# Optimization experiments

Hardware: AMD Instinct MI355X
Metric: run time of the kernel (lower is better)

The kernel has to match this reference:

```python
import jax, jax.numpy as jnp
import numpy as np
import math

N, S, D, V = 8, 2048, 64, 64

def setup_inputs() -> dict:
    key = jax.random.key(0)
    k1, k2, k3, k4 = jax.random.split(key, 4)
    return {
        "queries_nqd": jax.random.normal(k1, (N, S, D), dtype=jnp.float32),
        "keys_nsd": jax.random.normal(k2, (N, S, D), dtype=jnp.float32),
        "values_nsv": jax.random.normal(k3, (N, S, V), dtype=jnp.float32),
        "prefix_len_n": jax.random.randint(k4, (N,), 0, S, dtype=jnp.int64) if jax.config.jax_enable_x64 else jax.random.randint(k4, (N,), 0, S, dtype=jnp.int32),
    }

def reference(queries_nqd, keys_nsd, values_nsv, prefix_len_n):
    n, q, d = queries_nqd.shape
    s = keys_nsd.shape[1]
    # block mask: key position < prefix_len (broadcast over query dim)  [n, q, s]
    s_idx = jnp.arange(s)
    block_mask = s_idx[None, None, :] < prefix_len_n[:, None, None]
    # diagonal mask: q == s index  [q, s]
    diag_mask = s_idx[:, None] == s_idx[None, :]
    attention_mask_nqs = block_mask | diag_mask[None, :, :]
    scores_nqs = jnp.einsum("nqd,nsd->nqs", queries_nqd, keys_nsd) / math.sqrt(d)
    scores_nqs = jnp.where(attention_mask_nqs, scores_nqs, jnp.float32(-1e9))
    probs_nqs = jax.nn.softmax(scores_nqs, axis=-1)
    # dropout p=0.0 (eval/identity)
    return jnp.einsum("nqs,nsv->nqv", probs_nqs, values_nsv)
```

## Files before the change

kernel.cpp:

```cpp
#include <hip/hip_runtime.h>
#include <cstdint>
#include <cstddef>

typedef __attribute__((ext_vector_type(8))) __bf16 bf16x8;
typedef __attribute__((ext_vector_type(2))) __bf16 bf16x2;
typedef __attribute__((ext_vector_type(4))) float f32x4;
typedef __attribute__((ext_vector_type(4))) unsigned int u32x4;

#define LOG2E 1.44269504088896340736f

constexpr int N_ = 8;
constexpr int S_ = 2048;
constexpr int D_ = 64;
constexpr int V_ = 64;
constexpr int TQ = 16;
constexpr int CK = 64;
constexpr int NW = 4;

#define GLD(d, a, OFF) \
    asm volatile("global_load_dwordx4 %0, %1, off offset:" OFF : "=&v"(d) : "v"(a))
#define VDRAIN() do { asm volatile("s_waitcnt vmcnt(0)" ::: "memory"); \
                      __builtin_amdgcn_sched_barrier(0); } while (0)

__device__ __forceinline__ ushort f2bf(float x) {
    uint u = __builtin_bit_cast(uint, x);
    return (ushort)((u + 0x7FFFu + ((u >> 16) & 1u)) >> 16);
}
__device__ __forceinline__ bf16x8 bc8(const u32x4& q) {
    return __builtin_bit_cast(bf16x8, q);
}
__device__ __forceinline__ bf16x8 cvt8(const float* p, float sc) {
    f32x4 a = *reinterpret_cast<const f32x4*>(p);
    f32x4 b = *reinterpret_cast<const f32x4*>(p + 4);
    bf16x8 r;
#pragma unroll
    for (int j = 0; j < 4; j++) { r[j] = (__bf16)(a[j] * sc); r[j + 4] = (__bf16)(b[j] * sc); }
    return r;
}
__device__ __forceinline__ uint pk2(float lo, float hi) {
    bf16x2 t; t[0] = (__bf16)lo; t[1] = (__bf16)hi;
    return __builtin_bit_cast(uint, t);
}

__device__ __forceinline__ int load_prefix(const int* plen, int n) {
    bool is64 = ((plen[1] | plen[3] | plen[5] | plen[7]) == 0);
    return is64 ? plen[2 * n] : plen[n];
}

__global__ void prep_kernel(const float* __restrict__ Q, const float* __restrict__ K,
                            const float* __restrict__ V, ushort* __restrict__ Qb,
                            ushort* __restrict__ Kb, ushort* __restrict__ VTb) {
    const float QS = 0.125f * LOG2E;
    const int i4 = (blockIdx.x * 256 + threadIdx.x) * 4;
    f32x4 q = *reinterpret_cast<const f32x4*>(Q + i4);
    f32x4 k = *reinterpret_cast<const f32x4*>(K + i4);
    f32x4 v = *reinterpret_cast<const f32x4*>(V + i4);
    ushort4 qo, ko;
    qo.x = f2bf(q[0] * QS); qo.y = f2bf(q[1] * QS); qo.z = f2bf(q[2] * QS); qo.w = f2bf(q[3] * QS);
    ko.x = f2bf(k[0]); ko.y = f2bf(k[1]); ko.z = f2bf(k[2]); ko.w = f2bf(k[3]);
    *reinterpret_cast<ushort4*>(Qb + i4) = qo;
    *reinterpret_cast<ushort4*>(Kb + i4) = ko;
    const int vd = i4 & (V_ - 1);
    const int s  = (i4 >> 6) & (S_ - 1);
    const int n  = i4 >> 17;
    const size_t base = ((size_t)n * 64 + (s >> 5)) * 2048 + (s & 31);
#pragma unroll
    for (int j = 0; j < 4; j++)
        VTb[base + (size_t)(vd + j) * 32] = f2bf(v[j]);
}

template <bool WS>
__global__ __launch_bounds__(256, 2) void attn_kernel(
    const void* __restrict__ Qp, const void* __restrict__ Kp,
    const void* __restrict__ Vp, const ushort* __restrict__ VTb,
    const int* __restrict__ plen, float* __restrict__ outm)
{
    __shared__ float obuf[NW][TQ][V_ + 1];
    __shared__ float lbuf[NW][TQ];

    const int n    = blockIdx.y;
    const int q0   = blockIdx.x * TQ;
    const int tid  = threadIdx.x;
    const int w    = tid >> 6;
    const int lane = tid & 63;
    const int quad = lane >> 4;
    const int l16  = lane & 15;
    const int prefix = load_prefix(plen, n);
    const int qrow = q0 + l16;

    const int krow = ((l16 >> 2) << 3) + (l16 & 3);

    bf16x8 qf0, qf1;
    if (WS) {
        const ushort* qptr = (const ushort*)Qp + ((size_t)(n * S_ + qrow)) * D_ + quad * 8;
        uint4 u0 = *reinterpret_cast<const uint4*>(qptr);
        uint4 u1 = *reinterpret_cast<const uint4*>(qptr + 32);
        qf0 = __builtin_bit_cast(bf16x8, u0); qf1 = __builtin_bit_cast(bf16x8, u1);
    } else {
        const float* qptr = (const float*)Qp + ((size_t)(n * S_ + qrow)) * D_ + quad * 8;
        qf0 = cvt8(qptr, 0.125f * LOG2E); qf1 = cvt8(qptr + 32, 0.125f * LOG2E);
    }

    f32x4 oacc[4];
#pragma unroll
    for (int vb = 0; vb < 4; vb++) oacc[vb] = (f32x4){0.f, 0.f, 0.f, 0.f};
    float l_r = 0.f;

    const float* Kf = (const float*)Kp + (size_t)n * S_ * D_;
    const float* Vf = (const float*)Vp + (size_t)n * S_ * V_;

    const uint64_t kbase0 = (uint64_t)(uintptr_t)((const ushort*)Kp)
        + (size_t)n * S_ * D_ * 2 + (size_t)krow * 128 + quad * 16;
    const uint64_t vbase0 = (uint64_t)(uintptr_t)VTb
        + (size_t)n * 64 * 2048 * 2 + (size_t)l16 * 64 + quad * 16;

    auto issueKV = [&](u32x4* f, int c) {
        const uint64_t ka = kbase0 + (uint64_t)c * (CK * 128);
        const uint64_t kb = ka + 4096;
        const uint64_t va = vbase0 + (uint64_t)c * (2 * 4096);
        const uint64_t vb = va + 4096;
        GLD(f[0],  ka, "0");   GLD(f[1],  ka, "64");
        GLD(f[2],  ka, "512"); GLD(f[3],  ka, "576");
        GLD(f[4],  kb, "0");   GLD(f[5],  kb, "64");
        GLD(f[6],  kb, "512"); GLD(f[7],  kb, "576");
        GLD(f[8],  va, "0");   GLD(f[9],  va, "1024");
        GLD(f[10], va, "2048");GLD(f[11], va, "3072");
        GLD(f[12], vb, "0");   GLD(f[13], vb, "1024");
        GLD(f[14], vb, "2048");GLD(f[15], vb, "3072");
    };

    auto computeKV = [&](const u32x4* f, int kb, bool masked) {
        const f32x4 zero = (f32x4){0.f, 0.f, 0.f, 0.f};
        f32x4 s0 = __builtin_amdgcn_mfma_f32_16x16x32_bf16(bc8(f[0]), qf0, zero, 0, 0, 0);
        s0 = __builtin_amdgcn_mfma_f32_16x16x32_bf16(bc8(f[1]), qf1, s0, 0, 0, 0);
        f32x4 s1 = __builtin_amdgcn_mfma_f32_16x16x32_bf16(bc8(f[2]), qf0, zero, 0, 0, 0);
        s1 = __builtin_amdgcn_mfma_f32_16x16x32_bf16(bc8(f[3]), qf1, s1, 0, 0, 0);
        f32x4 s2 = __builtin_amdgcn_mfma_f32_16x16x32_bf16(bc8(f[4]), qf0, zero, 0, 0, 0);
        s2 = __builtin_amdgcn_mfma_f32_16x16x32_bf16(bc8(f[5]), qf1, s2, 0, 0, 0);
        f32x4 s3 = __builtin_amdgcn_mfma_f32_16x16x32_bf16(bc8(f[6]), qf0, zero, 0, 0, 0);
        s3 = __builtin_amdgcn_mfma_f32_16x16x32_bf16(bc8(f[7]), qf1, s3, 0, 0, 0);
        if (masked) {
#pragma unroll
            for (int r = 0; r < 4; r++) {
                const int k0 = kb + 8 * quad + r;
                s0[r] = (k0      < prefix || k0      == qrow) ? s0[r] : -1e30f;
                s1[r] = (k0 + 4  < prefix || k0 + 4  == qrow) ? s1[r] : -1e30f;
                s2[r] = (k0 + 32 < prefix || k0 + 32 == qrow) ? s2[r] : -1e30f;
                s3[r] = (k0 + 36 < prefix || k0 + 36 == qrow) ? s3[r] : -1e30f;
            }
        }
        float p0[4], p1[4], p2[4], p3[4];
#pragma unroll
        for (int r = 0; r < 4; r++) {
            p0[r] = __builtin_amdgcn_exp2f(s0[r]);
            p1[r] = __builtin_amdgcn_exp2f(s1[r]);
            p2[r] = __builtin_amdgcn_exp2f(s2[r]);
            p3[r] = __builtin_amdgcn_exp2f(s3[r]);
        }
        l_r += ((p0[0] + p0[1]) + (p0[2] + p0[3])) + ((p1[0] + p1[1]) + (p1[2] + p1[3]))
             + ((p2[0] + p2[1]) + (p2[2] + p2[3])) + ((p3[0] + p3[1]) + (p3[2] + p3[3]));
        uint4 pw0, pw1;
        pw0.x = pk2(p0[0], p0[1]); pw0.y = pk2(p0[2], p0[3]);
        pw0.z = pk2(p1[0], p1[1]); pw0.w = pk2(p1[2], p1[3]);
        pw1.x = pk2(p2[0], p2[1]); pw1.y = pk2(p2[2], p2[3]);
        pw1.z = pk2(p3[0], p3[1]); pw1.w = pk2(p3[2], p3[3]);
        const bf16x8 pB0 = __builtin_bit_cast(bf16x8, pw0);
        const bf16x8 pB1 = __builtin_bit_cast(bf16x8, pw1);
#pragma unroll
        for (int vb = 0; vb < 4; vb++) {
            oacc[vb] = __builtin_amdgcn_mfma_f32_16x16x32_bf16(bc8(f[8 + vb]),  pB0, oacc[vb], 0, 0, 0);
            oacc[vb] = __builtin_amdgcn_mfma_f32_16x16x32_bf16(bc8(f[12 + vb]), pB1, oacc[vb], 0, 0, 0);
        }
    };

    auto computeNW = [&](int kb, bool masked) {
        const f32x4 zero = (f32x4){0.f, 0.f, 0.f, 0.f};
        const float* kp = Kf + (size_t)(kb + krow) * D_ + quad * 8;
        bf16x8 k0a = cvt8(kp, 1.f),           k0b = cvt8(kp + 32, 1.f);
        bf16x8 k1a = cvt8(kp + 4 * D_, 1.f),  k1b = cvt8(kp + 4 * D_ + 32, 1.f);
        bf16x8 k2a = cvt8(kp + 32 * D_, 1.f), k2b = cvt8(kp + 32 * D_ + 32, 1.f);
        bf16x8 k3a = cvt8(kp + 36 * D_, 1.f), k3b = cvt8(kp + 36 * D_ + 32, 1.f);
        f32x4 s0 = __builtin_amdgcn_mfma_f32_16x16x32_bf16(k0a, qf0, zero, 0, 0, 0);
        s0 = __builtin_amdgcn_mfma_f32_16x16x32_bf16(k0b, qf1, s0, 0, 0, 0);
        f32x4 s1 = __builtin_amdgcn_mfma_f32_16x16x32_bf16(k1a, qf0, zero, 0, 0, 0);
        s1 = __builtin_amdgcn_mfma_f32_16x16x32_bf16(k1b, qf1, s1, 0, 0, 0);
        f32x4 s2 = __builtin_amdgcn_mfma_f32_16x16x32_bf16(k2a, qf0, zero, 0, 0, 0);
        s2 = __builtin_amdgcn_mfma_f32_16x16x32_bf16(k2b, qf1, s2, 0, 0, 0);
        f32x4 s3 = __builtin_amdgcn_mfma_f32_16x16x32_bf16(k3a, qf0, zero, 0, 0, 0);
        s3 = __builtin_amdgcn_mfma_f32_16x16x32_bf16(k3b, qf1, s3, 0, 0, 0);
        if (masked) {
#pragma unroll
            for (int r = 0; r < 4; r++) {
                const int k0 = kb + 8 * quad + r;
                s0[r] = (k0      < prefix || k0      == qrow) ? s0[r] : -1e30f;
                s1[r] = (k0 + 4  < prefix || k0 + 4  == qrow) ? s1[r] : -1e30f;
                s2[r] = (k0 + 32 < prefix || k0 + 32 == qrow) ? s2[r] : -1e30f;
                s3[r] = (k0 + 36 < prefix || k0 + 36 == qrow) ? s3[r] : -1e30f;
            }
        }
        float p0[4], p1[4], p2[4], p3[4];
#pragma unroll
        for (int r = 0; r < 4; r++) {
            p0[r] = __builtin_amdgcn_exp2f(s0[r]);
            p1[r] = __builtin_amdgcn_exp2f(s1[r]);
            p2[r] = __builtin_amdgcn_exp2f(s2[r]);
            p3[r] = __builtin_amdgcn_exp2f(s3[r]);
        }
        l_r += ((p0[0] + p0[1]) + (p0[2] + p0[3])) + ((p1[0] + p1[1]) + (p1[2] + p1[3]))
             + ((p2[0] + p2[1]) + (p2[2] + p2[3])) + ((p3[0] + p3[1]) + (p3[2] + p3[3]));
        uint4 pw0, pw1;
        pw0.x = pk2(p0[0], p0[1]); pw0.y = pk2(p0[2], p0[3]);
        pw0.z = pk2(p1[0], p1[1]); pw0.w = pk2(p1[2], p1[3]);
        pw1.x = pk2(p2[0], p2[1]); pw1.y = pk2(p2[2], p2[3]);
        pw1.z = pk2(p3[0], p3[1]); pw1.w = pk2(p3[2], p3[3]);
        const bf16x8 pB0 = __builtin_bit_cast(bf16x8, pw0);
        const bf16x8 pB1 = __builtin_bit_cast(bf16x8, pw1);
#pragma unroll
        for (int vb = 0; vb < 4; vb++) {
            bf16x8 vf0, vf1;
#pragma unroll
            for (int j = 0; j < 8; j++) {
                vf0[j] = (__bf16)Vf[(size_t)(kb + quad * 8 + j) * V_ + vb * 16 + l16];
                vf1[j] = (__bf16)Vf[(size_t)(kb + 32 + quad * 8 + j) * V_ + vb * 16 + l16];
            }
            oacc[vb] = __builtin_amdgcn_mfma_f32_16x16x32_bf16(vf0, pB0, oacc[vb], 0, 0, 0);
            oacc[vb] = __builtin_amdgcn_mfma_f32_16x16x32_bf16(vf1, pB1, oacc[vb], 0, 0, 0);
        }
    };

    const int nFull = prefix >> 6;
    const int nPC   = (prefix + CK - 1) >> 6;
    const int dc    = q0 >> 6;

    if (WS) {
        u32x4 bufA[16], bufB[16];
        int c = w;
        if (c < nFull) {
            issueKV(bufA, c);
            VDRAIN();
            for (;;) {
                int cn = c + NW;
                if (cn >= nFull) { computeKV(bufA, c * CK, false); break; }
                issueKV(bufB, cn);
                computeKV(bufA, c * CK, false);
                VDRAIN();
                c = cn; cn = c + NW;
                if (cn >= nFull) { computeKV(bufB, c * CK, false); break; }
                issueKV(bufA, cn);
                computeKV(bufB, c * CK, false);
                VDRAIN();
                c = cn;
            }
        }
        if (nPC > nFull && (nFull & (NW - 1)) == w) {
            issueKV(bufA, nFull); VDRAIN(); computeKV(bufA, nFull * CK, true);
        }
        if (dc >= nPC && (dc & (NW - 1)) == w) {
            issueKV(bufA, dc); VDRAIN(); computeKV(bufA, dc * CK, true);
        }
    } else {
        for (int c = w; c < nFull; c += NW) computeNW(c * CK, false);
        if (nPC > nFull && (nFull & (NW - 1)) == w) computeNW(nFull * CK, true);
        if (dc >= nPC && (dc & (NW - 1)) == w) computeNW(dc * CK, true);
    }

#pragma unroll
    for (int vb = 0; vb < 4; vb++)
#pragma unroll
        for (int r = 0; r < 4; r++)
            obuf[w][l16][vb * 16 + quad * 4 + r] = oacc[vb][r];
    l_r += __shfl_xor(l_r, 16, 64);
    l_r += __shfl_xor(l_r, 32, 64);
    if (quad == 0) lbuf[w][l16] = l_r;
    __syncthreads();

    const int row = tid >> 4;
    const int vd0 = (tid & 15) * 4;
    float lg = (lbuf[0][row] + lbuf[1][row]) + (lbuf[2][row] + lbuf[3][row]);
    float acc[4] = {0.f, 0.f, 0.f, 0.f};
#pragma unroll
    for (int ww = 0; ww < NW; ww++) {
#pragma unroll
        for (int i = 0; i < 4; i++) acc[i] += obuf[ww][row][vd0 + i];
    }
    const float inv = 1.f / lg;
    f32x4 o4 = (f32x4){acc[0] * inv, acc[1] * inv, acc[2] * inv, acc[3] * inv};
    *reinterpret_cast<f32x4*>(outm + ((size_t)(n * S_ + q0 + row)) * V_ + vd0) = o4;
}

extern "C" void kernel_launch(void* const* d_in, const int* in_sizes, int n_in,
                              void* d_out, int out_size, void* d_ws, size_t ws_size,
                              hipStream_t stream) {
    const float* Qf = (const float*)d_in[0];
    const float* Kf = (const float*)d_in[1];
    const float* Vf = (const float*)d_in[2];
    const int* plen = (const int*)d_in[3];
    float* outm = (float*)d_out;

    constexpr size_t ELEMS = (size_t)N_ * S_ * D_;
    const size_t need = 3 * ELEMS * sizeof(ushort);
    dim3 agrid(S_ / TQ, N_);

    if (ws_size >= need) {
        ushort* Qb  = (ushort*)d_ws;
        ushort* Kb  = Qb + ELEMS;
        ushort* VTb = Kb + ELEMS;
        prep_kernel<<<ELEMS / (256 * 4), 256, 0, stream>>>(Qf, Kf, Vf, Qb, Kb, VTb);
        attn_kernel<true><<<agrid, 256, 0, stream>>>(Qb, Kb, nullptr, VTb, plen, outm);
    } else {
        attn_kernel<false><<<agrid, 256, 0, stream>>>(Qf, Kf, Vf, nullptr, plen, outm);
    }
}
```

Measured before the change: 101.3 us.

## Process two query tiles per warp and overlap K/V loads with partial waits

Doubles the query tile to 32 rows so each warp runs two 16-row score/PV MFMA streams over the same K/V fragments. This halves K/V global traffic per query and halves the grid. It also replaces full vmcnt drains with partial waits (vmcnt 24/16), so V loads and the next chunk's prefetch can overlap the QK computation. In exchange, register pressure is higher, there are fewer blocks to balance the uneven prefix lengths, and a dead no-op loop is left in the fallback path.

```diff
diff --git a/kernel.cpp b/kernel.cpp
--- a/kernel.cpp
+++ b/kernel.cpp
@@ -13,13 +13,13 @@
 constexpr int S_ = 2048;
 constexpr int D_ = 64;
 constexpr int V_ = 64;
-constexpr int TQ = 16;
+constexpr int TQ = 32;
 constexpr int CK = 64;
 constexpr int NW = 4;
 
 #define GLD(d, a, OFF) \
     asm volatile("global_load_dwordx4 %0, %1, off offset:" OFF : "=&v"(d) : "v"(a))
-#define VDRAIN() do { asm volatile("s_waitcnt vmcnt(0)" ::: "memory"); \
+#define WAITV(N) do { asm volatile("s_waitcnt vmcnt(" #N ")" ::: "memory"); \
                       __builtin_amdgcn_sched_barrier(0); } while (0)
 
 __device__ __forceinline__ ushort f2bf(float x) {
@@ -86,25 +86,31 @@
     const int quad = lane >> 4;
     const int l16  = lane & 15;
     const int prefix = load_prefix(plen, n);
-    const int qrow = q0 + l16;
+    const int qrow0 = q0 + l16;
+    const int qrow1 = q0 + 16 + l16;
 
     const int krow = ((l16 >> 2) << 3) + (l16 & 3);
 
-    bf16x8 qf0, qf1;
+    bf16x8 qf00, qf01, qf10, qf11;
     if (WS) {
-        const ushort* qptr = (const ushort*)Qp + ((size_t)(n * S_ + qrow)) * D_ + quad * 8;
+        const ushort* qptr = (const ushort*)Qp + ((size_t)(n * S_ + qrow0)) * D_ + quad * 8;
         uint4 u0 = *reinterpret_cast<const uint4*>(qptr);
         uint4 u1 = *reinterpret_cast<const uint4*>(qptr + 32);
-        qf0 = __builtin_bit_cast(bf16x8, u0); qf1 = __builtin_bit_cast(bf16x8, u1);
+        uint4 u2 = *reinterpret_cast<const uint4*>(qptr + 16 * D_);
+        uint4 u3 = *reinterpret_cast<const uint4*>(qptr + 16 * D_ + 32);
+        qf00 = __builtin_bit_cast(bf16x8, u0); qf01 = __builtin_bit_cast(bf16x8, u1);
+        qf10 = __builtin_bit_cast(bf16x8, u2); qf11 = __builtin_bit_cast(bf16x8, u3);
     } else {
-        const float* qptr = (const float*)Qp + ((size_t)(n * S_ + qrow)) * D_ + quad * 8;
-        qf0 = cvt8(qptr, 0.125f * LOG2E); qf1 = cvt8(qptr + 32, 0.125f * LOG2E);
+        const float* qptr = (const float*)Qp + ((size_t)(n * S_ + qrow0)) * D_ + quad * 8;
+        qf00 = cvt8(qptr, 0.125f * LOG2E);            qf01 = cvt8(qptr + 32, 0.125f * LOG2E);
+        qf10 = cvt8(qptr + 16 * D_, 0.125f * LOG2E);  qf11 = cvt8(qptr + 16 * D_ + 32, 0.125f * LOG2E);
     }
-
-    f32x4 oacc[4];
-#pragma unroll
-    for (int vb = 0; vb < 4; vb++) oacc[vb] = (f32x4){0.f, 0.f, 0.f, 0.f};
-    float l_r = 0.f;
+    asm volatile("" : "+v"(qf00), "+v"(qf01), "+v"(qf10), "+v"(qf11));
+
+    f32x4 oa[4], ob[4];
+#pragma unroll
+    for (int vb = 0; vb < 4; vb++) { oa[vb] = (f32x4){0.f,0.f,0.f,0.f}; ob[vb] = (f32x4){0.f,0.f,0.f,0.f}; }
+    float l0 = 0.f, l1 = 0.f;
 
     const float* Kf = (const float*)Kp + (size_t)n * S_ * D_;
     const float* Vf = (const float*)Vp + (size_t)n * S_ * V_;
@@ -129,102 +135,88 @@
         GLD(f[14], vb, "2048");GLD(f[15], vb, "3072");
     };
 
-    auto computeKV = [&](const u32x4* f, int kb, bool masked) {
+    auto computeChunk = [&](const u32x4* f, int kb, bool masked, bool wait16) {
         const f32x4 zero = (f32x4){0.f, 0.f, 0.f, 0.f};
-        f32x4 s0 = __builtin_amdgcn_mfma_f32_16x16x32_bf16(bc8(f[0]), qf0, zero, 0, 0, 0);
-        s0 = __builtin_amdgcn_mfma_f32_16x16x32_bf16(bc8(f[1]), qf1, s0, 0, 0, 0);
-        f32x4 s1 = __builtin_amdgcn_mfma_f32_16x16x32_bf16(bc8(f[2]), qf0, zero, 0, 0, 0);
-        s1 = __builtin_amdgcn_mfma_f32_16x16x32_bf16(bc8(f[3]), qf1, s1, 0, 0, 0);
-        f32x4 s2 = __builtin_amdgcn_mfma_f32_16x16x32_bf16(bc8(f[4]), qf0, zero, 0, 0, 0);
-        s2 = __builtin_amdgcn_mfma_f32_16x16x32_bf16(bc8(f[5]), qf1, s2, 0, 0, 0);
-        f32x4 s3 = __builtin_amdgcn_mfma_f32_16x16x32_bf16(bc8(f[6]), qf0, zero, 0, 0, 0);
-        s3 = __builtin_amdgcn_mfma_f32_16x16x32_bf16(bc8(f[7]), qf1, s3, 0, 0, 0);
-        if (masked) {
+        uint4 pw0, pw1, pw2, pw3;
+        {
+            f32x4 s0 = __builtin_amdgcn_mfma_f32_16x16x32_bf16(bc8(f[0]), qf00, zero, 0, 0, 0);
+            s0 = __builtin_amdgcn_mfma_f32_16x16x32_bf16(bc8(f[1]), qf01, s0, 0, 0, 0);
+            f32x4 s1 = __builtin_amdgcn_mfma_f32_16x16x32_bf16(bc8(f[2]), qf00, zero, 0, 0, 0);
+            s1 = __builtin_amdgcn_mfma_f32_16x16x32_bf16(bc8(f[3]), qf01, s1, 0, 0, 0);
+            f32x4 s2 = __builtin_amdgcn_mfma_f32_16x16x32_bf16(bc8(f[4]), qf00, zero, 0, 0, 0);
+            s2 = __builtin_amdgcn_mfma_f32_16x16x32_bf16(bc8(f[5]), qf01, s2, 0, 0, 0);
+            f32x4 s3 = __builtin_amdgcn_mfma_f32_16x16x32_bf16(bc8(f[6]), qf00, zero, 0, 0, 0);
+            s3 = __builtin_amdgcn_mfma_f32_16x16x32_bf16(bc8(f[7]), qf01, s3, 0, 0, 0);
+            if (masked) {
+#pragma unroll
+                for (int r = 0; r < 4; r++) {
+                    const int k0 = kb + 8 * quad + r;
+                    s0[r] = (k0      < prefix || k0      == qrow0) ? s0[r] : -1e30f;
+                    s1[r] = (k0 + 4  < prefix || k0 + 4  == qrow0) ? s1[r] : -1e30f;
+                    s2[r] = (k0 + 32 < prefix || k0 + 32 == qrow0) ? s2[r] : -1e30f;
+                    s3[r] = (k0 + 36 < prefix || k0 + 36 == qrow0) ? s3[r] : -1e30f;
+                }
+            }
+            float p0[4], p1[4], p2[4], p3[4];
 #pragma unroll
             for (int r = 0; r < 4; r++) {
-                const int k0 = kb + 8 * quad + r;
-                s0[r] = (k0      < prefix || k0      == qrow) ? s0[r] : -1e30f;
-                s1[r] = (k0 + 4  < prefix || k0 + 4  == qrow) ? s1[r] : -1e30f;
-                s2[r] = (k0 + 32 < prefix || k0 + 32 == qrow) ? s2[r] : -1e30f;
-                s3[r] = (k0 + 36 < prefix || k0 + 36 == qrow) ? s3[r] : -1e30f;
-            }
-        }
-        float p0[4], p1[4], p2[4], p3[4];
-#pragma unroll
-        for (int r = 0; r < 4; r++) {
-            p0[r] = __builtin_amdgcn_exp2f(s0[r]);
-            p1[r] = __builtin_amdgcn_exp2f(s1[r]);
-            p2[r] = __builtin_amdgcn_exp2f(s2[r]);
-            p3[r] = __builtin_amdgcn_exp2f(s3[r]);
-        }
-        l_r += ((p0[0] + p0[1]) + (p0[2] + p0[3])) + ((p1[0] + p1[1]) + (p1[2] + p1[3]))
-             + ((p2[0] + p2[1]) + (p2[2] + p2[3])) + ((p3[0] + p3[1]) + (p3[2] + p3[3]));
-        uint4 pw0, pw1;
-        pw0.x = pk2(p0[0], p0[1]); pw0.y = pk2(p0[2], p0[3]);
-        pw0.z = pk2(p1[0], p1[1]); pw0.w = pk2(p1[2], p1[3]);
-        pw1.x = pk2(p2[0], p2[1]); pw1.y = pk2(p2[2], p2[3]);
-        pw1.z = pk2(p3[0], p3[1]); pw1.w = pk2(p3[2], p3[3]);
-        const bf16x8 pB0 = __builtin_bit_cast(bf16x8, pw0);
-        const bf16x8 pB1 = __builtin_bit_cast(bf16x8, pw1);
+                p0[r] = __builtin_amdgcn_exp2f(s0[r]);
+                p1[r] = __builtin_amdgcn_exp2f(s1[r]);
+                p2[r] = __builtin_amdgcn_exp2f(s2[r]);
+                p3[r] = __builtin_amdgcn_exp2f(s3[r]);
+            }
+            l0 += ((p0[0]+p0[1])+(p0[2]+p0[3])) + ((p1[0]+p1[1])+(p1[2]+p1[3]))
+                + ((p2[0]+p2[1])+(p2[2]+p2[3])) + ((p3[0]+p3[1])+(p3[2]+p3[3]));
+            pw0.x = pk2(p0[0], p0[1]); pw0.y = pk2(p0[2], p0[3]);
+            pw0.z = pk2(p1[0], p1[1]); pw0.w = pk2(p1[2], p1[3]);
+            pw1.x = pk2(p2[0], p2[1]); pw1.y = pk2(p2[2], p2[3]);
+            pw1.z = pk2(p3[0], p3[1]); pw1.w = pk2(p3[2], p3[3]);
+        }
+        {
+            f32x4 s0 = __builtin_amdgcn_mfma_f32_16x16x32_bf16(bc8(f[0]), qf10, zero, 0, 0, 0);
+            s0 = __builtin_amdgcn_mfma_f32_16x16x32_bf16(bc8(f[1]), qf11, s0, 0, 0, 0);
+            f32x4 s1 = __builtin_amdgcn_mfma_f32_16x16x32_bf16(bc8(f[2]), qf10, zero, 0, 0, 0);
+            s1 = __builtin_amdgcn_mfma_f32_16x16x32_bf16(bc8(f[3]), qf11, s1, 0, 0, 0);
+            f32x4 s2 = __builtin_amdgcn_mfma_f32_16x16x32_bf16(bc8(f[4]), qf10, zero, 0, 0, 0);
+            s2 = __builtin_amdgcn_mfma_f32_16x16x32_bf16(bc8(f[5]), qf11, s2, 0, 0, 0);
+            f32x4 s3 = __builtin_amdgcn_mfma_f32_16x16x32_bf16(bc8(f[6]), qf10, zero, 0, 0, 0);
+            s3 = __builtin_amdgcn_mfma_f32_16x16x32_bf16(bc8(f[7]), qf11, s3, 0, 0, 0);
+            if (masked) {
+#pragma unroll
+                for (int r = 0; r < 4; r++) {
+                    const int k0 = kb + 8 * quad + r;
+                    s0[r] = (k0      < prefix || k0      == qrow1) ? s0[r] : -1e30f;
+                    s1[r] = (k0 + 4  < prefix || k0 + 4  == qrow1) ? s1[r] : -1e30f;
+                    s2[r] = (k0 + 32 < prefix || k0 + 32 == qrow1) ? s2[r] : -1e30f;
+                    s3[r] = (k0 + 36 < prefix || k0 + 36 == qrow1) ? s3[r] : -1e30f;
+                }
+            }
+            float p0[4], p1[4], p2[4], p3[4];
+#pragma unroll
+            for (int r = 0; r < 4; r++) {
+                p0[r] = __builtin_amdgcn_exp2f(s0[r]);
+                p1[r] = __builtin_amdgcn_exp2f(s1[r]);
+                p2[r] = __builtin_amdgcn_exp2f(s2[r]);
+                p3[r] = __builtin_amdgcn_exp2f(s3[r]);
+            }
+            l1 += ((p0[0]+p0[1])+(p0[2]+p0[3])) + ((p1[0]+p1[1])+(p1[2]+p1[3]))
+                + ((p2[0]+p2[1])+(p2[2]+p2[3])) + ((p3[0]+p3[1])+(p3[2]+p3[3]));
+            pw2.x = pk2(p0[0], p0[1]); pw2.y = pk2(p0[2], p0[3]);
+            pw2.z = pk2(p1[0], p1[1]); pw2.w = pk2(p1[2], p1[3]);
+            pw3.x = pk2(p2[0], p2[1]); pw3.y = pk2(p2[2], p2[3]);
+            pw3.z = pk2(p3[0], p3[1]); pw3.w = pk2(p3[2], p3[3]);
+        }
+        if (wait16) WAITV(16);
+        const bf16x8 pA0 = __builtin_bit_cast(bf16x8, pw0);
+        const bf16x8 pA1 = __builtin_bit_cast(bf16x8, pw1);
+        const bf16x8 pB0 = __builtin_bit_cast(bf16x8, pw2);
+        const bf16x8 pB1 = __builtin_bit_cast(bf16x8, pw3);
 #pragma unroll
         for (int vb = 0; vb < 4; vb++) {
-            oacc[vb] = __builtin_amdgcn_mfma_f32_16x16x32_bf16(bc8(f[8 + vb]),  pB0, oacc[vb], 0, 0, 0);
-            oacc[vb] = __builtin_amdgcn_mfma_f32_16x16x32_bf16(bc8(f[12 + vb]), pB1, oacc[vb], 0, 0, 0);
-        }
-    };
-
-    auto computeNW = [&](int kb, bool masked) {
-        const f32x4 zero = (f32x4){0.f, 0.f, 0.f, 0.f};
-        const float* kp = Kf + (size_t)(kb + krow) * D_ + quad * 8;
-        bf16x8 k0a = cvt8(kp, 1.f),           k0b = cvt8(kp + 32, 1.f);
-        bf16x8 k1a = cvt8(kp + 4 * D_, 1.f),  k1b = cvt8(kp + 4 * D_ + 32, 1.f);
-        bf16x8 k2a = cvt8(kp + 32 * D_, 1.f), k2b = cvt8(kp + 32 * D_ + 32, 1.f);
-        bf16x8 k3a = cvt8(kp + 36 * D_, 1.f), k3b = cvt8(kp + 36 * D_ + 32, 1.f);
-        f32x4 s0 = __builtin_amdgcn_mfma_f32_16x16x32_bf16(k0a, qf0, zero, 0, 0, 0);
-        s0 = __builtin_amdgcn_mfma_f32_16x16x32_bf16(k0b, qf1, s0, 0, 0, 0);
-        f32x4 s1 = __builtin_amdgcn_mfma_f32_16x16x32_bf16(k1a, qf0, zero, 0, 0, 0);
-        s1 = __builtin_amdgcn_mfma_f32_16x16x32_bf16(k1b, qf1, s1, 0, 0, 0);
-        f32x4 s2 = __builtin_amdgcn_mfma_f32_16x16x32_bf16(k2a, qf0, zero, 0, 0, 0);
-        s2 = __builtin_amdgcn_mfma_f32_16x16x32_bf16(k2b, qf1, s2, 0, 0, 0);
-        f32x4 s3 = __builtin_amdgcn_mfma_f32_16x16x32_bf16(k3a, qf0, zero, 0, 0, 0);
-        s3 = __builtin_amdgcn_mfma_f32_16x16x32_bf16(k3b, qf1, s3, 0, 0, 0);
-        if (masked) {
-#pragma unroll
-            for (int r = 0; r < 4; r++) {
-                const int k0 = kb + 8 * quad + r;
-                s0[r] = (k0      < prefix || k0      == qrow) ? s0[r] : -1e30f;
-                s1[r] = (k0 + 4  < prefix || k0 + 4  == qrow) ? s1[r] : -1e30f;
-                s2[r] = (k0 + 32 < prefix || k0 + 32 == qrow) ? s2[r] : -1e30f;
-                s3[r] = (k0 + 36 < prefix || k0 + 36 == qrow) ? s3[r] : -1e30f;
-            }
-        }
-        float p0[4], p1[4], p2[4], p3[4];
-#pragma unroll
-        for (int r = 0; r < 4; r++) {
-            p0[r] = __builtin_amdgcn_exp2f(s0[r]);
-            p1[r] = __builtin_amdgcn_exp2f(s1[r]);
-            p2[r] = __builtin_amdgcn_exp2f(s2[r]);
-            p3[r] = __builtin_amdgcn_exp2f(s3[r]);
-        }
-        l_r += ((p0[0] + p0[1]) + (p0[2] + p0[3])) + ((p1[0] + p1[1]) + (p1[2] + p1[3]))
-             + ((p2[0] + p2[1]) + (p2[2] + p2[3])) + ((p3[0] + p3[1]) + (p3[2] + p3[3]));
-        uint4 pw0, pw1;
-        pw0.x = pk2(p0[0], p0[1]); pw0.y = pk2(p0[2], p0[3]);
-        pw0.z = pk2(p1[0], p1[1]); pw0.w = pk2(p1[2], p1[3]);
-        pw1.x = pk2(p2[0], p2[1]); pw1.y = pk2(p2[2], p2[3]);
-        pw1.z = pk2(p3[0], p3[1]); pw1.w = pk2(p3[2], p3[3]);
-        const bf16x8 pB0 = __builtin_bit_cast(bf16x8, pw0);
-        const bf16x8 pB1 = __builtin_bit_cast(bf16x8, pw1);
-#pragma unroll
-        for (int vb = 0; vb < 4; vb++) {
-            bf16x8 vf0, vf1;
-#pragma unroll
-            for (int j = 0; j < 8; j++) {
-                vf0[j] = (__bf16)Vf[(size_t)(kb + quad * 8 + j) * V_ + vb * 16 + l16];
-                vf1[j] = (__bf16)Vf[(size_t)(kb + 32 + quad * 8 + j) * V_ + vb * 16 + l16];
-            }
-            oacc[vb] = __builtin_amdgcn_mfma_f32_16x16x32_bf16(vf0, pB0, oacc[vb], 0, 0, 0);
-            oacc[vb] = __builtin_amdgcn_mfma_f32_16x16x32_bf16(vf1, pB1, oacc[vb], 0, 0, 0);
+            oa[vb] = __builtin_amdgcn_mfma_f32_16x16x32_bf16(bc8(f[8 + vb]),  pA0, oa[vb], 0, 0, 0);
+            oa[vb] = __builtin_amdgcn_mfma_f32_16x16x32_bf16(bc8(f[12 + vb]), pA1, oa[vb], 0, 0, 0);
+            ob[vb] = __builtin_amdgcn_mfma_f32_16x16x32_bf16(bc8(f[8 + vb]),  pB0, ob[vb], 0, 0, 0);
+            ob[vb] = __builtin_amdgcn_mfma_f32_16x16x32_bf16(bc8(f[12 + vb]), pB1, ob[vb], 0, 0, 0);
         }
     };
 
@@ -237,28 +229,70 @@
         int c = w;
         if (c < nFull) {
             issueKV(bufA, c);
-            VDRAIN();
-            for (;;) {
-                int cn = c + NW;
-                if (cn >= nFull) { computeKV(bufA, c * CK, false); break; }
-                issueKV(bufB, cn);
-                computeKV(bufA, c * CK, false);
-                VDRAIN();
-                c = cn; cn = c + NW;
-                if (cn >= nFull) { computeKV(bufB, c * CK, false); break; }
-                issueKV(bufA, cn);
-                computeKV(bufB, c * CK, false);
-                VDRAIN();
-                c = cn;
+            int c1 = c + NW;
+            if (c1 >= nFull) {
+                WAITV(0); computeChunk(bufA, c * CK, false, false);
+            } else {
+                issueKV(bufB, c1);
+                for (;;) {
+                    int c2 = c1 + NW;
+                    if (c2 >= nFull) {
+                        WAITV(16); computeChunk(bufA, c * CK, false, false);
+                        WAITV(0);  computeChunk(bufB, c1 * CK, false, false);
+                        break;
+                    }
+                    WAITV(24);
+                    computeChunk(bufA, c * CK, false, true);
+                    issueKV(bufA, c2);
+                    c = c1; c1 = c2; c2 = c1 + NW;
+                    if (c2 >= nFull) {
+                        WAITV(16); computeChunk(bufB, c * CK, false, false);
+                        WAITV(0);  computeChunk(bufA, c1 * CK, false, false);
+                        break;
+                    }
+                    WAITV(24);
+                    computeChunk(bufB, c * CK, false, true);
+                    issueKV(bufB, c2);
+                    c = c1; c1 = c2;
+                }
             }
         }
         if (nPC > nFull && (nFull & (NW - 1)) == w) {
-            issueKV(bufA, nFull); VDRAIN(); computeKV(bufA, nFull * CK, true);
+            issueKV(bufA, nFull); WAITV(0); computeChunk(bufA, nFull * CK, true, false);
         }
         if (dc >= nPC && (dc & (NW - 1)) == w) {
-            issueKV(bufA, dc); VDRAIN(); computeKV(bufA, dc * CK, true);
+            issueKV(bufA, dc); WAITV(0); computeChunk(bufA, dc * CK, true, false);
         }
     } else {
+        for (int c = w; c < nFull + 2; c++) {
+            int cc; bool masked;
+            if (c < nFull) { if ((c & (NW - 1)) != (w & (NW - 1)) || c >= nFull) {} }
+            break;
+        }
+        auto computeNW = [&](int kb, bool masked) {
+            u32x4 f[16];
+            const float* kp = Kf + (size_t)(kb + krow) * D_ + quad * 8;
+            f[0] = __builtin_bit_cast(u32x4, cvt8(kp, 1.f));
+            f[1] = __builtin_bit_cast(u32x4, cvt8(kp + 32, 1.f));
+            f[2] = __builtin_bit_cast(u32x4, cvt8(kp + 4 * D_, 1.f));
+            f[3] = __builtin_bit_cast(u32x4, cvt8(kp + 4 * D_ + 32, 1.f));
+            f[4] = __builtin_bit_cast(u32x4, cvt8(kp + 32 * D_, 1.f));
+            f[5] = __builtin_bit_cast(u32x4, cvt8(kp + 32 * D_ + 32, 1.f));
+            f[6] = __builtin_bit_cast(u32x4, cvt8(kp + 36 * D_, 1.f));
+            f[7] = __builtin_bit_cast(u32x4, cvt8(kp + 36 * D_ + 32, 1.f));
+#pragma unroll
+            for (int vb = 0; vb < 4; vb++) {
+                bf16x8 vf0, vf1;
+#pragma unroll
+                for (int j = 0; j < 8; j++) {
+                    vf0[j] = (__bf16)Vf[(size_t)(kb + quad * 8 + j) * V_ + vb * 16 + l16];
+                    vf1[j] = (__bf16)Vf[(size_t)(kb + 32 + quad * 8 + j) * V_ + vb * 16 + l16];
+                }
+                f[8 + vb]  = __builtin_bit_cast(u32x4, vf0);
+                f[12 + vb] = __builtin_bit_cast(u32x4, vf1);
+            }
+            computeChunk(f, kb, masked, false);
+        };
         for (int c = w; c < nFull; c += NW) computeNW(c * CK, false);
         if (nPC > nFull && (nFull & (NW - 1)) == w) computeNW(nFull * CK, true);
         if (dc >= nPC && (dc & (NW - 1)) == w) computeNW(dc * CK, true);
@@ -267,25 +301,32 @@
 #pragma unroll
     for (int vb = 0; vb < 4; vb++)
 #pragma unroll
-        for (int r = 0; r < 4; r++)
-            obuf[w][l16][vb * 16 + quad * 4 + r] = oacc[vb][r];
-    l_r += __shfl_xor(l_r, 16, 64);
-    l_r += __shfl_xor(l_r, 32, 64);
-    if (quad == 0) lbuf[w][l16] = l_r;
+        for (int r = 0; r < 4; r++) {
+            obuf[w][l16][vb * 16 + quad * 4 + r]      = oa[vb][r];
+            obuf[w][16 + l16][vb * 16 + quad * 4 + r] = ob[vb][r];
+        }
+    l0 += __shfl_xor(l0, 16, 64);
+    l0 += __shfl_xor(l0, 32, 64);
+    l1 += __shfl_xor(l1, 16, 64);
+    l1 += __shfl_xor(l1, 32, 64);
+    if (quad == 0) { lbuf[w][l16] = l0; lbuf[w][16 + l16] = l1; }
     __syncthreads();
 
-    const int row = tid >> 4;
-    const int vd0 = (tid & 15) * 4;
+    const int row = tid >> 3;
+    const int vd0 = (tid & 7) * 8;
     float lg = (lbuf[0][row] + lbuf[1][row]) + (lbuf[2][row] + lbuf[3][row]);
-    float acc[4] = {0.f, 0.f, 0.f, 0.f};
+    float acc[8] = {0.f,0.f,0.f,0.f,0.f,0.f,0.f,0.f};
 #pragma unroll
     for (int ww = 0; ww < NW; ww++) {
 #pragma unroll
-        for (int i = 0; i < 4; i++) acc[i] += obuf[ww][row][vd0 + i];
+        for (int i = 0; i < 8; i++) acc[i] += obuf[ww][row][vd0 + i];
     }
     const float inv = 1.f / lg;
-    f32x4 o4 = (f32x4){acc[0] * inv, acc[1] * inv, acc[2] * inv, acc[3] * inv};
-    *reinterpret_cast<f32x4*>(outm + ((size_t)(n * S_ + q0 + row)) * V_ + vd0) = o4;
+    f32x4 o4a = (f32x4){acc[0] * inv, acc[1] * inv, acc[2] * inv, acc[3] * inv};
+    f32x4 o4b = (f32x4){acc[4] * inv, acc[5] * inv, acc[6] * inv, acc[7] * inv};
+    float* op = outm + ((size_t)(n * S_ + q0 + row)) * V_ + vd0;
+    *reinterpret_cast<f32x4*>(op)     = o4a;
+    *reinterpret_cast<f32x4*>(op + 4) = o4b;
 }
 
 extern "C" void kernel_launch(void* const* d_in, const int* in_sizes, int n_in,
```

Result: faster. 91.46 us (-9.7%).
